# Kernel tuning notes

Hardware: AMD Instinct MI355X
Metric: run time of the kernel (lower is better)

Reference implementation:

```python
import jax, jax.numpy as jnp
import numpy as np

B, N, H, OUT, VOCAB = 1024, 128, 64, 128, 117


def setup_inputs() -> dict:
    key = jax.random.key(0)
    k_g, k_a, k_e, k1, k2, k3 = jax.random.split(key, 6)
    graph = jax.random.randint(k_g, (B, N), 0, VOCAB, dtype=jnp.int64 if jax.config.jax_enable_x64 else jnp.int32)
    adj = jax.random.uniform(k_a, (B, N, N), dtype=jnp.float32)
    # learned params: embedding table + per-layer GraphLinear weights (torch Linear: [out,in], no bias)
    embed = jax.random.normal(k_e, (VOCAB, H), dtype=jnp.float32) * 0.02
    s = 1.0 / np.sqrt(H)
    W1 = jax.random.uniform(k1, (H, H), minval=-s, maxval=s, dtype=jnp.float32)
    W2 = jax.random.uniform(k2, (H, H), minval=-s, maxval=s, dtype=jnp.float32)
    W3 = jax.random.uniform(k3, (OUT, H), minval=-s, maxval=s, dtype=jnp.float32)
    return {"graph": graph, "adj": adj, "embed": embed, "W1": W1, "W2": W2, "W3": W3}


def reference(graph, adj, embed, W1, W2, W3):
    # h: [B, N, H] atom embeddings
    h = embed[graph]
    weights = (W1, W2, W3)
    n_layers = len(weights)
    for i, W in enumerate(weights):
        # message passing: adj @ h, then per-node linear (no bias): x @ W^T
        h = jnp.einsum('bij,bjd->bid', adj, h)
        h = jnp.einsum('bnd,od->bno', h, W)
        if i < n_layers - 1:
            h = jax.nn.relu(h)
    # sum readout over atoms -> [B, OUT]
    return jnp.sum(h, axis=1)
```

## Files before the change

### kernel.cpp

```cpp
#include <hip/hip_runtime.h>

typedef __bf16 bf16x8 __attribute__((ext_vector_type(8)));
typedef float  f32x4  __attribute__((ext_vector_type(4)));

#define NB 1024
#define NN 128
#define NH 64
#define NOUT 128

__device__ __forceinline__ unsigned short f2b(float f) {
    return __builtin_bit_cast(unsigned short, (__bf16)f);
}

__global__ __launch_bounds__(256, 2)
void rsgcn_fused(const int* __restrict__ graph, const float* __restrict__ adj,
                 const float* __restrict__ embed, const float* __restrict__ W1,
                 const float* __restrict__ W2, const float* __restrict__ W3,
                 float* __restrict__ out)
{
    __shared__ __align__(16) char smem[65536];
    char* const adj_s = smem;
    char* const hT_s  = smem + 32768;
    char* const S_s   = smem + 49152;
    float* const part   = (float*)S_s;
    float* const colsum = (float*)S_s;
    float* const svec   = (float*)(S_s + 512);

    const int b    = blockIdx.x;
    const int t    = threadIdx.x;
    const int lane = t & 63;
    const int wv   = t >> 6;

    const float4* adj4 = (const float4*)(adj + (size_t)b * (NN * NN));
    {
        float p0 = 0.f, p1 = 0.f, p2 = 0.f, p3 = 0.f;
        #pragma unroll
        for (int i = 0; i < 16; ++i) {
            int fi = i * 256 + t;
            float4 v = adj4[fi];
            p0 += v.x; p1 += v.y; p2 += v.z; p3 += v.w;
            int row  = fi >> 5;
            int colb = (fi & 31) * 8;
            ushort4 u;
            u.x = f2b(v.x); u.y = f2b(v.y); u.z = f2b(v.z); u.w = f2b(v.w);
            *(ushort4*)(adj_s + row * 256 + (colb ^ ((row & 7) << 4))) = u;
        }
        *(float4*)(part + t * 4) = make_float4(p0, p1, p2, p3);
    }

    {
        const int j  = t >> 1;
        const int d0 = (t & 1) * 32;
        const int g  = graph[b * NN + j];
        const float4* erow = (const float4*)(embed + g * NH + d0);
        #pragma unroll
        for (int q = 0; q < 8; ++q) {
            float4 v = erow[q];
            int d = d0 + q * 4;
            *(unsigned short*)(hT_s + (d+0)*256 + ((j*2) ^ (((d+0)&7)<<4))) = f2b(v.x);
            *(unsigned short*)(hT_s + (d+1)*256 + ((j*2) ^ (((d+1)&7)<<4))) = f2b(v.y);
            *(unsigned short*)(hT_s + (d+2)*256 + ((j*2) ^ (((d+2)&7)<<4))) = f2b(v.z);
            *(unsigned short*)(hT_s + (d+3)*256 + ((j*2) ^ (((d+3)&7)<<4))) = f2b(v.w);
        }
    }
    __syncthreads();

    float cs = 0.f;
    if (t < 128) {
        #pragma unroll
        for (int k = 0; k < 8; ++k)
            cs += part[(((t >> 2) + 32 * k) << 2) + (t & 3)];
    }
    __syncthreads();

    #pragma unroll 1
    for (int layer = 0; layer < 2; ++layer) {
        const float* W = (layer == 0) ? W1 : W2;

        {
            f32x4 acc[2][4] = {};
            const int r0  = (2 * wv) * 16 + (lane & 15);
            const int r1  = r0 + 16;
            const int kb0 = (lane >> 4) * 16;
            #pragma unroll
            for (int kk = 0; kk < 4; ++kk) {
                int kb = kk * 64 + kb0;
                bf16x8 a0 = *(const bf16x8*)(adj_s + r0*256 + (kb ^ ((r0 & 7) << 4)));
                bf16x8 a1 = *(const bf16x8*)(adj_s + r1*256 + (kb ^ ((r1 & 7) << 4)));
                #pragma unroll
                for (int nt = 0; nt < 4; ++nt) {
                    int rh = nt * 16 + (lane & 15);
                    bf16x8 bb = *(const bf16x8*)(hT_s + rh*256 + (kb ^ ((rh & 7) << 4)));
                    acc[0][nt] = __builtin_amdgcn_mfma_f32_16x16x32_bf16(a0, bb, acc[0][nt], 0, 0, 0);
                    acc[1][nt] = __builtin_amdgcn_mfma_f32_16x16x32_bf16(a1, bb, acc[1][nt], 0, 0, 0);
                }
            }
            #pragma unroll
            for (int m = 0; m < 2; ++m) {
                #pragma unroll
                for (int nt = 0; nt < 4; ++nt) {
                    #pragma unroll
                    for (int i = 0; i < 4; ++i) {
                        int node = (2*wv + m) * 16 + (lane >> 4) * 4 + i;
                        int d    = nt * 16 + (lane & 15);
                        *(unsigned short*)(S_s + node*128 + ((d*2) ^ ((node & 7) << 4))) =
                            f2b(acc[m][nt][i]);
                    }
                }
            }
        }
        __syncthreads();

        {
            bf16x8 aw[2];
            const int o = wv * 16 + (lane & 15);
            #pragma unroll
            for (int kk = 0; kk < 2; ++kk) {
                int d = kk * 32 + (lane >> 4) * 8;
                const float4* p = (const float4*)(W + o * NH + d);
                float4 v0 = p[0], v1 = p[1];
                bf16x8 a;
                a[0] = (__bf16)v0.x; a[1] = (__bf16)v0.y; a[2] = (__bf16)v0.z; a[3] = (__bf16)v0.w;
                a[4] = (__bf16)v1.x; a[5] = (__bf16)v1.y; a[6] = (__bf16)v1.z; a[7] = (__bf16)v1.w;
                aw[kk] = a;
            }
            f32x4 acc2[8] = {};
            #pragma unroll
            for (int kk = 0; kk < 2; ++kk) {
                int db = kk * 64 + (lane >> 4) * 16;
                #pragma unroll
                for (int nt = 0; nt < 8; ++nt) {
                    int rn = nt * 16 + (lane & 15);
                    bf16x8 bb = *(const bf16x8*)(S_s + rn*128 + (db ^ ((rn & 7) << 4)));
                    acc2[nt] = __builtin_amdgcn_mfma_f32_16x16x32_bf16(aw[kk], bb, acc2[nt], 0, 0, 0);
                }
            }
            __syncthreads();
            #pragma unroll
            for (int nt = 0; nt < 8; ++nt) {
                #pragma unroll
                for (int i = 0; i < 4; ++i) {
                    int oo   = wv * 16 + (lane >> 4) * 4 + i;
                    int node = nt * 16 + (lane & 15);
                    float v = acc2[nt][i];
                    v = fmaxf(v, 0.0f);
                    *(unsigned short*)(hT_s + oo*256 + ((node*2) ^ ((oo & 7) << 4))) = f2b(v);
                }
            }
        }
        __syncthreads();
    }

    if (t < 128) colsum[t] = cs;
    __syncthreads();

    if (t < 64) {
        float s0 = 0.f, s1 = 0.f;
        #pragma unroll
        for (int jj = 0; jj < 16; ++jj) {
            bf16x8 hv = *(const bf16x8*)(hT_s + t*256 + ((jj*16) ^ ((t & 7) << 4)));
            float q0 = 0.f, q1 = 0.f;
            #pragma unroll
            for (int q = 0; q < 4; ++q) {
                q0 += colsum[jj*8 + q]     * (float)hv[q];
                q1 += colsum[jj*8 + 4 + q] * (float)hv[4 + q];
            }
            s0 += q0; s1 += q1;
        }
        svec[t] = s0 + s1;
    }
    __syncthreads();

    if (t < 128) {
        const float4* wrow = (const float4*)(W3 + t * NH);
        float a0 = 0.f, a1 = 0.f;
        #pragma unroll
        for (int q = 0; q < 16; q += 2) {
            float4 w0 = wrow[q], w1 = wrow[q + 1];
            a0 += w0.x*svec[q*4+0] + w0.y*svec[q*4+1] + w0.z*svec[q*4+2] + w0.w*svec[q*4+3];
            a1 += w1.x*svec[q*4+4] + w1.y*svec[q*4+5] + w1.z*svec[q*4+6] + w1.w*svec[q*4+7];
        }
        out[b * NOUT + t] = a0 + a1;
    }
}

extern "C" void kernel_launch(void* const* d_in, const int* in_sizes, int n_in,
                              void* d_out, int out_size, void* d_ws, size_t ws_size,
                              hipStream_t stream) {
    const int*   graph = (const int*)d_in[0];
    const float* adjp  = (const float*)d_in[1];
    const float* embed = (const float*)d_in[2];
    const float* W1    = (const float*)d_in[3];
    const float* W2    = (const float*)d_in[4];
    const float* W3    = (const float*)d_in[5];
    float* outp = (float*)d_out;

    rsgcn_fused<<<dim3(NB), dim3(256), 0, stream>>>(graph, adjp, embed, W1, W2, W3, outp);
}
```

Measured before the change: 32.61 us.

## Use 512-thread blocks, preload adj/embed to registers, hoist weight fragments

Doubles the block to 512 threads (8 waves) and re-partitions the adj@h MFMA work so each wave computes a 16x64 tile, computing it transposed (h^T @ adj^T) so results land as packed ushort4 stores. All adj and embedding loads are issued up front into registers before the LDS writes, and the embedding transpose is written as vectorised 4-node packs. W1/W2 bf16 fragments are loaded once before the layer loop instead of per layer, and the final colsum-weighted reduction uses all threads with shuffle reductions. The goal is more memory-level parallelism and more waves per CU to hide the adjacency load latency, at the cost of higher register pressure and 64KB LDS per block, which may limit occupancy.

```diff
diff --git a/kernel.cpp b/kernel.cpp
--- a/kernel.cpp
+++ b/kernel.cpp
@@ -12,7 +12,7 @@
     return __builtin_bit_cast(unsigned short, (__bf16)f);
 }
 
-__global__ __launch_bounds__(256, 2)
+__global__ __launch_bounds__(512, 4)
 void rsgcn_fused(const int* __restrict__ graph, const float* __restrict__ adj,
                  const float* __restrict__ embed, const float* __restrict__ W1,
                  const float* __restrict__ W2, const float* __restrict__ W3,
@@ -31,16 +31,29 @@
     const int lane = t & 63;
     const int wv   = t >> 6;
 
+    const int jq = t & 31;
+    const int dq = t >> 5;
+    const int d0 = dq * 4;
+    const int4 g4 = *(const int4*)(graph + b * NN + jq * 4);
+
     const float4* adj4 = (const float4*)(adj + (size_t)b * (NN * NN));
+    float4 av[8];
+    #pragma unroll
+    for (int i = 0; i < 8; ++i) av[i] = adj4[i * 512 + t];
+
+    float4 e0 = *(const float4*)(embed + g4.x * NH + d0);
+    float4 e1 = *(const float4*)(embed + g4.y * NH + d0);
+    float4 e2 = *(const float4*)(embed + g4.z * NH + d0);
+    float4 e3 = *(const float4*)(embed + g4.w * NH + d0);
+
     {
         float p0 = 0.f, p1 = 0.f, p2 = 0.f, p3 = 0.f;
         #pragma unroll
-        for (int i = 0; i < 16; ++i) {
-            int fi = i * 256 + t;
-            float4 v = adj4[fi];
+        for (int i = 0; i < 8; ++i) {
+            float4 v = av[i];
             p0 += v.x; p1 += v.y; p2 += v.z; p3 += v.w;
-            int row  = fi >> 5;
-            int colb = (fi & 31) * 8;
+            int row  = i * 16 + dq;
+            int colb = jq * 8;
             ushort4 u;
             u.x = f2b(v.x); u.y = f2b(v.y); u.z = f2b(v.z); u.w = f2b(v.w);
             *(ushort4*)(adj_s + row * 256 + (colb ^ ((row & 7) << 4))) = u;
@@ -49,103 +62,99 @@
     }
 
     {
-        const int j  = t >> 1;
-        const int d0 = (t & 1) * 32;
-        const int g  = graph[b * NN + j];
-        const float4* erow = (const float4*)(embed + g * NH + d0);
-        #pragma unroll
-        for (int q = 0; q < 8; ++q) {
-            float4 v = erow[q];
-            int d = d0 + q * 4;
-            *(unsigned short*)(hT_s + (d+0)*256 + ((j*2) ^ (((d+0)&7)<<4))) = f2b(v.x);
-            *(unsigned short*)(hT_s + (d+1)*256 + ((j*2) ^ (((d+1)&7)<<4))) = f2b(v.y);
-            *(unsigned short*)(hT_s + (d+2)*256 + ((j*2) ^ (((d+2)&7)<<4))) = f2b(v.z);
-            *(unsigned short*)(hT_s + (d+3)*256 + ((j*2) ^ (((d+3)&7)<<4))) = f2b(v.w);
-        }
-    }
-    __syncthreads();
-
-    float cs = 0.f;
-    if (t < 128) {
-        #pragma unroll
-        for (int k = 0; k < 8; ++k)
-            cs += part[(((t >> 2) + 32 * k) << 2) + (t & 3)];
-    }
-    __syncthreads();
-
-    #pragma unroll 1
-    for (int layer = 0; layer < 2; ++layer) {
-        const float* W = (layer == 0) ? W1 : W2;
-
-        {
-            f32x4 acc[2][4] = {};
-            const int r0  = (2 * wv) * 16 + (lane & 15);
-            const int r1  = r0 + 16;
-            const int kb0 = (lane >> 4) * 16;
-            #pragma unroll
-            for (int kk = 0; kk < 4; ++kk) {
-                int kb = kk * 64 + kb0;
-                bf16x8 a0 = *(const bf16x8*)(adj_s + r0*256 + (kb ^ ((r0 & 7) << 4)));
-                bf16x8 a1 = *(const bf16x8*)(adj_s + r1*256 + (kb ^ ((r1 & 7) << 4)));
-                #pragma unroll
-                for (int nt = 0; nt < 4; ++nt) {
-                    int rh = nt * 16 + (lane & 15);
-                    bf16x8 bb = *(const bf16x8*)(hT_s + rh*256 + (kb ^ ((rh & 7) << 4)));
-                    acc[0][nt] = __builtin_amdgcn_mfma_f32_16x16x32_bf16(a0, bb, acc[0][nt], 0, 0, 0);
-                    acc[1][nt] = __builtin_amdgcn_mfma_f32_16x16x32_bf16(a1, bb, acc[1][nt], 0, 0, 0);
-                }
-            }
-            #pragma unroll
-            for (int m = 0; m < 2; ++m) {
-                #pragma unroll
-                for (int nt = 0; nt < 4; ++nt) {
-                    #pragma unroll
-                    for (int i = 0; i < 4; ++i) {
-                        int node = (2*wv + m) * 16 + (lane >> 4) * 4 + i;
-                        int d    = nt * 16 + (lane & 15);
-                        *(unsigned short*)(S_s + node*128 + ((d*2) ^ ((node & 7) << 4))) =
-                            f2b(acc[m][nt][i]);
-                    }
-                }
-            }
-        }
-        __syncthreads();
-
-        {
-            bf16x8 aw[2];
-            const int o = wv * 16 + (lane & 15);
+        float ea[4][4];
+        *(float4*)ea[0] = e0; *(float4*)ea[1] = e1;
+        *(float4*)ea[2] = e2; *(float4*)ea[3] = e3;
+        #pragma unroll
+        for (int k = 0; k < 4; ++k) {
+            int d = d0 + k;
+            ushort4 u;
+            u.x = f2b(ea[0][k]); u.y = f2b(ea[1][k]);
+            u.z = f2b(ea[2][k]); u.w = f2b(ea[3][k]);
+            *(ushort4*)(hT_s + d * 256 + ((jq * 8) ^ ((d & 7) << 4))) = u;
+        }
+    }
+
+    bf16x8 wf[2][8];
+    #pragma unroll
+    for (int L = 0; L < 2; ++L) {
+        const float* W = L ? W2 : W1;
+        #pragma unroll
+        for (int nt = 0; nt < 4; ++nt) {
             #pragma unroll
             for (int kk = 0; kk < 2; ++kk) {
-                int d = kk * 32 + (lane >> 4) * 8;
-                const float4* p = (const float4*)(W + o * NH + d);
+                const float4* p = (const float4*)(W + (nt * 16 + (lane & 15)) * NH
+                                                  + kk * 32 + (lane >> 4) * 8);
                 float4 v0 = p[0], v1 = p[1];
                 bf16x8 a;
                 a[0] = (__bf16)v0.x; a[1] = (__bf16)v0.y; a[2] = (__bf16)v0.z; a[3] = (__bf16)v0.w;
                 a[4] = (__bf16)v1.x; a[5] = (__bf16)v1.y; a[6] = (__bf16)v1.z; a[7] = (__bf16)v1.w;
-                aw[kk] = a;
-            }
-            f32x4 acc2[8] = {};
+                wf[L][nt * 2 + kk] = a;
+            }
+        }
+    }
+    __syncthreads();
+
+    float cs = 0.f;
+    if (t < 128) {
+        #pragma unroll
+        for (int k = 0; k < 16; ++k)
+            cs += part[(k * 32 + (t >> 2)) * 4 + (t & 3)];
+    }
+    __syncthreads();
+
+    const int mtA  = wv & 3;
+    const int ntA0 = (wv >> 2) * 4;
+    #pragma unroll
+    for (int layer = 0; layer < 2; ++layer) {
+        {
+            f32x4 acc[4] = {};
+            const int arow = mtA * 16 + (lane & 15);
+            const int koff = (lane >> 4) * 16;
+            #pragma unroll
+            for (int kk = 0; kk < 4; ++kk) {
+                int kb = kk * 64 + koff;
+                bf16x8 af = *(const bf16x8*)(hT_s + arow * 256 + (kb ^ ((arow & 7) << 4)));
+                #pragma unroll
+                for (int nt = 0; nt < 4; ++nt) {
+                    int brow = (ntA0 + nt) * 16 + (lane & 15);
+                    bf16x8 bf = *(const bf16x8*)(adj_s + brow * 256 + (kb ^ ((brow & 7) << 4)));
+                    acc[nt] = __builtin_amdgcn_mfma_f32_16x16x32_bf16(af, bf, acc[nt], 0, 0, 0);
+                }
+            }
+            const int dd0 = mtA * 16 + (lane >> 4) * 4;
+            #pragma unroll
+            for (int nt = 0; nt < 4; ++nt) {
+                int node = (ntA0 + nt) * 16 + (lane & 15);
+                ushort4 u;
+                u.x = f2b(acc[nt][0]); u.y = f2b(acc[nt][1]);
+                u.z = f2b(acc[nt][2]); u.w = f2b(acc[nt][3]);
+                *(ushort4*)(S_s + node * 128 + ((dd0 * 2) ^ ((node & 7) << 4))) = u;
+            }
+        }
+        __syncthreads();
+
+        {
+            f32x4 acc[4] = {};
+            const int arow = wv * 16 + (lane & 15);
+            const int koff = (lane >> 4) * 16;
             #pragma unroll
             for (int kk = 0; kk < 2; ++kk) {
-                int db = kk * 64 + (lane >> 4) * 16;
+                int kb = kk * 64 + koff;
+                bf16x8 af = *(const bf16x8*)(S_s + arow * 128 + (kb ^ ((arow & 7) << 4)));
                 #pragma unroll
-                for (int nt = 0; nt < 8; ++nt) {
-                    int rn = nt * 16 + (lane & 15);
-                    bf16x8 bb = *(const bf16x8*)(S_s + rn*128 + (db ^ ((rn & 7) << 4)));
-                    acc2[nt] = __builtin_amdgcn_mfma_f32_16x16x32_bf16(aw[kk], bb, acc2[nt], 0, 0, 0);
-                }
-            }
-            __syncthreads();
-            #pragma unroll
-            for (int nt = 0; nt < 8; ++nt) {
-                #pragma unroll
-                for (int i = 0; i < 4; ++i) {
-                    int oo   = wv * 16 + (lane >> 4) * 4 + i;
-                    int node = nt * 16 + (lane & 15);
-                    float v = acc2[nt][i];
-                    v = fmaxf(v, 0.0f);
-                    *(unsigned short*)(hT_s + oo*256 + ((node*2) ^ ((oo & 7) << 4))) = f2b(v);
-                }
+                for (int nt = 0; nt < 4; ++nt)
+                    acc[nt] = __builtin_amdgcn_mfma_f32_16x16x32_bf16(af, wf[layer][nt * 2 + kk],
+                                                                      acc[nt], 0, 0, 0);
+            }
+            const int node0 = wv * 16 + (lane >> 4) * 4;
+            #pragma unroll
+            for (int nt = 0; nt < 4; ++nt) {
+                int dout = nt * 16 + (lane & 15);
+                ushort4 u;
+                u.x = f2b(fmaxf(acc[nt][0], 0.f)); u.y = f2b(fmaxf(acc[nt][1], 0.f));
+                u.z = f2b(fmaxf(acc[nt][2], 0.f)); u.w = f2b(fmaxf(acc[nt][3], 0.f));
+                *(ushort4*)(hT_s + dout * 256 + ((node0 * 2) ^ ((dout & 7) << 4))) = u;
             }
         }
         __syncthreads();
@@ -154,20 +163,21 @@
     if (t < 128) colsum[t] = cs;
     __syncthreads();
 
-    if (t < 64) {
-        float s0 = 0.f, s1 = 0.f;
-        #pragma unroll
-        for (int jj = 0; jj < 16; ++jj) {
-            bf16x8 hv = *(const bf16x8*)(hT_s + t*256 + ((jj*16) ^ ((t & 7) << 4)));
-            float q0 = 0.f, q1 = 0.f;
-            #pragma unroll
-            for (int q = 0; q < 4; ++q) {
-                q0 += colsum[jj*8 + q]     * (float)hv[q];
-                q1 += colsum[jj*8 + 4 + q] * (float)hv[4 + q];
-            }
-            s0 += q0; s1 += q1;
-        }
-        svec[t] = s0 + s1;
+    {
+        const int d  = t >> 3;
+        const int jj = t & 7;
+        const int sw = (d & 7) << 4;
+        bf16x8 h0 = *(const bf16x8*)(hT_s + d * 256 + ((jj * 32)      ^ sw));
+        bf16x8 h1 = *(const bf16x8*)(hT_s + d * 256 + ((jj * 32 + 16) ^ sw));
+        float p = 0.f;
+        #pragma unroll
+        for (int q = 0; q < 8; ++q) p += colsum[jj * 16 + q]     * (float)h0[q];
+        #pragma unroll
+        for (int q = 0; q < 8; ++q) p += colsum[jj * 16 + 8 + q] * (float)h1[q];
+        p += __shfl_xor(p, 1);
+        p += __shfl_xor(p, 2);
+        p += __shfl_xor(p, 4);
+        if (jj == 0) svec[d] = p;
     }
     __syncthreads();
 
@@ -195,5 +205,5 @@
     const float* W3    = (const float*)d_in[5];
     float* outp = (float*)d_out;
 
-    rsgcn_fused<<<dim3(NB), dim3(256), 0, stream>>>(graph, adjp, embed, W1, W2, W3, outp);
+    rsgcn_fused<<<dim3(NB), dim3(512), 0, stream>>>(graph, adjp, embed, W1, W2, W3, outp);
 }
```

Result: slower. 56.27 us (+72.5%).
